# Kernel optimization log

Hardware: AMD Instinct MI355X
Metric: run time of the kernel (lower is better)

## Reference

```python
import jax, jax.numpy as jnp
import numpy as np

HIDDEN = 2048
N_HEADS = 32
HEAD_DIM = HIDDEN // N_HEADS
CONV_K = 4
INTER = 5632  # 256*ceil(2048*4*2/3/256)
EPS = 1e-6


def _rms(x, w):
    return x * jax.lax.rsqrt(jnp.mean(x * x, axis=-1, keepdims=True) + EPS) * w


def _l2norm(x):
    n = jnp.sqrt(jnp.sum(x * x, axis=-1, keepdims=True))
    return x / jnp.maximum(n, 1e-12)


def _causal_dwconv(x, w):
    # x [B,T,C], w [C,K] depthwise causal conv (left pad K-1), matches conv1d(pad=K-1)[..., :T]
    C, K = w.shape
    xt = jnp.transpose(x, (0, 2, 1))  # [B,C,T]
    out = jax.lax.conv_general_dilated(
        xt, w[:, None, :], window_strides=(1,), padding=[(K - 1, 0)],
        feature_group_count=C, dimension_numbers=('NCH', 'OIH', 'NCH'))
    return jnp.transpose(out, (0, 2, 1))


def _delta_scan(k, q, v, beta):
    # k,q,v: [B,T,nh,hd]; beta: [B,T,nh]. Per-head state S [hd(v), hd(k)].
    B, T, nh, hd = k.shape
    km, qm, vm = (jnp.moveaxis(a, 1, 0) for a in (k, q, v))  # [T,B,nh,hd]
    bm = jnp.moveaxis(beta, 1, 0)  # [T,B,nh]

    def step(S, inp):
        kt, qt, vt, bt = inp
        err = jnp.einsum('bhvk,bhk->bhv', S, kt) - vt
        S = S - bt[..., None, None] * err[..., None] * kt[..., None, :]
        o = jnp.einsum('bhvk,bhk->bhv', S, qt)
        return S, o

    S0 = jnp.zeros((B, nh, hd, hd), k.dtype)
    S, o = jax.lax.scan(step, S0, (km, qm, vm, bm))
    return jnp.moveaxis(o, 0, 1), S


def setup_inputs() -> dict:
    key = jax.random.key(0)
    ks = jax.random.split(key, 12)
    s = 0.02
    d = {
        'hidden_states': jax.random.normal(ks[0], (1, 1024, HIDDEN), jnp.float32),
        'attn_norm_w': jnp.ones((HIDDEN,), jnp.float32),
        'Wq': jax.random.normal(ks[1], (HIDDEN, HIDDEN), jnp.float32) * s,
        'Wk': jax.random.normal(ks[2], (HIDDEN, HIDDEN), jnp.float32) * s,
        'Wv': jax.random.normal(ks[3], (HIDDEN, HIDDEN), jnp.float32) * s,
        'conv_q': jax.random.normal(ks[4], (HIDDEN, CONV_K), jnp.float32) * 0.1,
        'conv_k': jax.random.normal(ks[5], (HIDDEN, CONV_K), jnp.float32) * 0.1,
        'conv_v': jax.random.normal(ks[6], (HIDDEN, CONV_K), jnp.float32) * 0.1,
        'Wbeta': jax.random.normal(ks[7], (N_HEADS, HIDDEN), jnp.float32) * s,
        'out_norm_w': jnp.ones((HIDDEN,), jnp.float32),
        'Wout': jax.random.normal(ks[8], (HIDDEN, HIDDEN), jnp.float32) * s,
        'mlp_norm_w': jnp.ones((HIDDEN,), jnp.float32),
        'Wgate': jax.random.normal(ks[9], (INTER, HIDDEN), jnp.float32) * s,
        'Wup': jax.random.normal(ks[10], (INTER, HIDDEN), jnp.float32) * s,
        'Wdown': jax.random.normal(ks[11], (HIDDEN, INTER), jnp.float32) * s,
    }
    return d


def reference(hidden_states, attn_norm_w, Wq, Wk, Wv, conv_q, conv_k, conv_v,
              Wbeta, out_norm_w, Wout, mlp_norm_w, Wgate, Wup, Wdown):
    x = hidden_states
    B, T, H = x.shape
    nh, hd = N_HEADS, HEAD_DIM
    silu = jax.nn.silu

    # --- DeltaNet attention sub-block ---
    h = _rms(x, attn_norm_w)
    # proj -> causal depthwise conv -> SiLU (in conv helper) -> SiLU again (forward)
    q = silu(silu(_causal_dwconv(h @ Wq.T, conv_q)))
    k = silu(silu(_causal_dwconv(h @ Wk.T, conv_k)))
    v = silu(silu(_causal_dwconv(h @ Wv.T, conv_v)))
    q = _l2norm(q.reshape(B, T, nh, hd))
    k = _l2norm(k.reshape(B, T, nh, hd))
    v = v.reshape(B, T, nh, hd)
    beta = jax.nn.sigmoid(h @ Wbeta.T)  # [B,T,nh]

    o, memory_state = _delta_scan(k, q, v, beta)
    o = o.reshape(B, T, H)
    o = _rms(o, out_norm_w) @ Wout.T
    x = x + o

    # --- SwiGLU MLP sub-block ---
    h2 = _rms(x, mlp_norm_w)
    gate = h2 @ Wgate.T
    up = h2 @ Wup.T
    x = x + (silu(gate) * up) @ Wdown.T
    return x, memory_state
```

## Files before the change

### kernel.cpp

```cpp
#include <hip/hip_runtime.h>
#include <stdint.h>

typedef unsigned short u16;
typedef unsigned int u32;

#define T_SEQ 1024
#define HID   2048
#define NH    32
#define HD    64
#define NCHUNK 16
#define INTER 5632

typedef __attribute__((ext_vector_type(8))) short b16x8;
typedef __attribute__((ext_vector_type(4))) float f32x4;

__device__ inline float bf2f(u16 u) { union { u32 i; float f; } v; v.i = ((u32)u) << 16; return v.f; }
__device__ inline u16 f2bf(float f) {
  union { float f; u32 i; } v; v.f = f;
  u32 u = v.i;
  return (u16)((u + 0x7FFFu + ((u >> 16) & 1u)) >> 16);
}
__device__ inline float silu_f(float x) { return x / (1.f + __expf(-x)); }

typedef __attribute__((address_space(1))) const unsigned int as1_u32;
typedef __attribute__((address_space(3))) unsigned int as3_u32;
__device__ inline void gl_lds16(const void* g, void* l) {
  __builtin_amdgcn_global_load_lds((as1_u32*)g, (as3_u32*)l, 16, 0, 0);
}

__global__ __launch_bounds__(256) void k_cvt_all(
    const float* __restrict__ s0, const float* __restrict__ s1, const float* __restrict__ s2,
    const float* __restrict__ s3, const float* __restrict__ s4, const float* __restrict__ s5,
    const float* __restrict__ s6,
    u16* __restrict__ d0, u16* __restrict__ d1, u16* __restrict__ d2, u16* __restrict__ d3,
    u16* __restrict__ d4, u16* __restrict__ d5, u16* __restrict__ d6) {
  int z = blockIdx.y;
  int n4 = (z < 4) ? (HID * HID / 4) : (INTER * HID / 4);
  int i = blockIdx.x * 256 + threadIdx.x;
  if (i >= n4) return;
  const float* s = (z == 0) ? s0 : (z == 1) ? s1 : (z == 2) ? s2 : (z == 3) ? s3
                   : (z == 4) ? s4 : (z == 5) ? s5 : s6;
  u16* d = (z == 0) ? d0 : (z == 1) ? d1 : (z == 2) ? d2 : (z == 3) ? d3
           : (z == 4) ? d4 : (z == 5) ? d5 : d6;
  float4 v = ((const float4*)s)[i];
  u32 lo = (u32)f2bf(v.x) | ((u32)f2bf(v.y) << 16);
  u32 hi = (u32)f2bf(v.z) | ((u32)f2bf(v.w) << 16);
  ((uint2*)d)[i] = make_uint2(lo, hi);
}

__global__ __launch_bounds__(256) void k_rms(const float* __restrict__ x, const float* __restrict__ w,
                                             u16* __restrict__ out) {
  int row = blockIdx.x, tid = threadIdx.x;
  const float* xr = x + (size_t)row * HID;
  float4 v0 = ((const float4*)xr)[tid];
  float4 v1 = ((const float4*)xr)[tid + 256];
  float ss = v0.x * v0.x + v0.y * v0.y + v0.z * v0.z + v0.w * v0.w +
             v1.x * v1.x + v1.y * v1.y + v1.z * v1.z + v1.w * v1.w;
  for (int m = 32; m; m >>= 1) ss += __shfl_xor(ss, m, 64);
  __shared__ float wsum[4];
  if ((tid & 63) == 0) wsum[tid >> 6] = ss;
  __syncthreads();
  float tot = wsum[0] + wsum[1] + wsum[2] + wsum[3];
  float sc = rsqrtf(tot / (float)HID + 1e-6f);
  float4 w0 = ((const float4*)w)[tid];
  float4 w1 = ((const float4*)w)[tid + 256];
  u32 lo, hi;
  lo = (u32)f2bf(v0.x * sc * w0.x) | ((u32)f2bf(v0.y * sc * w0.y) << 16);
  hi = (u32)f2bf(v0.z * sc * w0.z) | ((u32)f2bf(v0.w * sc * w0.w) << 16);
  ((uint2*)out)[(size_t)row * 512 + tid] = make_uint2(lo, hi);
  lo = (u32)f2bf(v1.x * sc * w1.x) | ((u32)f2bf(v1.y * sc * w1.y) << 16);
  hi = (u32)f2bf(v1.z * sc * w1.z) | ((u32)f2bf(v1.w * sc * w1.w) << 16);
  ((uint2*)out)[(size_t)row * 512 + tid + 256] = make_uint2(lo, hi);
}

__global__ __launch_bounds__(256) void k_gemm_sk(
    const u16* __restrict__ A,
    const u16* __restrict__ B0, const u16* __restrict__ B1, const u16* __restrict__ B2,
    float* __restrict__ C0, float* __restrict__ C1, float* __restrict__ C2,
    const float* __restrict__ resid, int M, int N, int Kf, int KS, int nslice) {
  int mat = blockIdx.z / nslice, slice = blockIdx.z % nslice;
  const u16* Bp = (mat == 0) ? B0 : (mat == 1 ? B1 : B2);
  float* Cp = (mat == 0) ? C0 : (mat == 1 ? C1 : C2);
  __shared__ __align__(16) u16 As[128 * 32];
  __shared__ __align__(16) u16 Bs[128 * 32];
  int tid = threadIdx.x;
  int m0 = blockIdx.y * 128, n0 = blockIdx.x * 128;
  int lane = tid & 63, wv = tid >> 6, wr = wv >> 1, wc = wv & 1;
  int lrow = lane & 15, quad = lane >> 4;
  int lr = lane >> 2;
  int lc = (((lane & 3) ^ ((lr >> 1) & 3)) * 8);
  int xq = quad ^ ((lrow >> 1) & 3);
  f32x4 acc[4][4];
#pragma unroll
  for (int i = 0; i < 4; ++i)
#pragma unroll
    for (int j = 0; j < 4; ++j) acc[i][j] = (f32x4){0.f, 0.f, 0.f, 0.f};

  int kb = slice * KS, ke = kb + KS;
  for (int k0 = kb; k0 < ke; k0 += 32) {
    const u16* Ag = A + (size_t)(m0 + wv * 32) * Kf + k0;
    const u16* Bg = Bp + (size_t)(n0 + wv * 32) * Kf + k0;
    gl_lds16(Ag + (size_t)lr * Kf + lc,        &As[(wv * 32) * 32]);
    gl_lds16(Ag + (size_t)(16 + lr) * Kf + lc, &As[(wv * 32 + 16) * 32]);
    gl_lds16(Bg + (size_t)lr * Kf + lc,        &Bs[(wv * 32) * 32]);
    gl_lds16(Bg + (size_t)(16 + lr) * Kf + lc, &Bs[(wv * 32 + 16) * 32]);
    __syncthreads();
    b16x8 af[4], bfr[4];
#pragma unroll
    for (int i = 0; i < 4; ++i) af[i] = *(const b16x8*)&As[(wr * 64 + i * 16 + lrow) * 32 + xq * 8];
#pragma unroll
    for (int j = 0; j < 4; ++j) bfr[j] = *(const b16x8*)&Bs[(wc * 64 + j * 16 + lrow) * 32 + xq * 8];
#pragma unroll
    for (int i = 0; i < 4; ++i)
#pragma unroll
      for (int j = 0; j < 4; ++j)
        acc[i][j] = __builtin_amdgcn_mfma_f32_16x16x32_bf16(af[i], bfr[j], acc[i][j], 0, 0, 0);
    __syncthreads();
  }
#pragma unroll
  for (int i = 0; i < 4; ++i)
#pragma unroll
    for (int j = 0; j < 4; ++j)
#pragma unroll
      for (int r = 0; r < 4; ++r) {
        int row = m0 + wr * 64 + i * 16 + quad * 4 + r;
        int col = n0 + wc * 64 + j * 16 + lrow;
        float val = acc[i][j][r];
        if (slice == 0 && resid) val += resid[(size_t)row * N + col];
        atomicAdd(&Cp[(size_t)row * N + col], val);
      }
}

__global__ __launch_bounds__(256) void k_gemm_gu(
    const u16* __restrict__ A, const u16* __restrict__ Bg, const u16* __restrict__ Bu,
    u16* __restrict__ D) {
  __shared__ __align__(16) u16 As[128 * 32];
  __shared__ __align__(16) u16 Gs[128 * 32];
  __shared__ __align__(16) u16 Us[128 * 32];
  int tid = threadIdx.x;
  int m0 = blockIdx.y * 128, n0 = blockIdx.x * 128;
  int lane = tid & 63, wv = tid >> 6, wr = wv >> 1, wc = wv & 1;
  int lrow = lane & 15, quad = lane >> 4;
  int lr = lane >> 2;
  int lc = (((lane & 3) ^ ((lr >> 1) & 3)) * 8);
  int xq = quad ^ ((lrow >> 1) & 3);
  f32x4 ag[4][4], au[4][4];
#pragma unroll
  for (int i = 0; i < 4; ++i)
#pragma unroll
    for (int j = 0; j < 4; ++j) { ag[i][j] = (f32x4){0.f, 0.f, 0.f, 0.f}; au[i][j] = (f32x4){0.f, 0.f, 0.f, 0.f}; }

  for (int k0 = 0; k0 < HID; k0 += 32) {
    const u16* Ap = A + (size_t)(m0 + wv * 32) * HID + k0;
    const u16* Gp = Bg + (size_t)(n0 + wv * 32) * HID + k0;
    const u16* Up = Bu + (size_t)(n0 + wv * 32) * HID + k0;
    gl_lds16(Ap + (size_t)lr * HID + lc,        &As[(wv * 32) * 32]);
    gl_lds16(Ap + (size_t)(16 + lr) * HID + lc, &As[(wv * 32 + 16) * 32]);
    gl_lds16(Gp + (size_t)lr * HID + lc,        &Gs[(wv * 32) * 32]);
    gl_lds16(Gp + (size_t)(16 + lr) * HID + lc, &Gs[(wv * 32 + 16) * 32]);
    gl_lds16(Up + (size_t)lr * HID + lc,        &Us[(wv * 32) * 32]);
    gl_lds16(Up + (size_t)(16 + lr) * HID + lc, &Us[(wv * 32 + 16) * 32]);
    __syncthreads();
    b16x8 af[4], gf[4], uf[4];
#pragma unroll
    for (int i = 0; i < 4; ++i) af[i] = *(const b16x8*)&As[(wr * 64 + i * 16 + lrow) * 32 + xq * 8];
#pragma unroll
    for (int j = 0; j < 4; ++j) gf[j] = *(const b16x8*)&Gs[(wc * 64 + j * 16 + lrow) * 32 + xq * 8];
#pragma unroll
    for (int j = 0; j < 4; ++j) uf[j] = *(const b16x8*)&Us[(wc * 64 + j * 16 + lrow) * 32 + xq * 8];
#pragma unroll
    for (int i = 0; i < 4; ++i)
#pragma unroll
      for (int j = 0; j < 4; ++j) {
        ag[i][j] = __builtin_amdgcn_mfma_f32_16x16x32_bf16(af[i], gf[j], ag[i][j], 0, 0, 0);
        au[i][j] = __builtin_amdgcn_mfma_f32_16x16x32_bf16(af[i], uf[j], au[i][j], 0, 0, 0);
      }
    __syncthreads();
  }
#pragma unroll
  for (int i = 0; i < 4; ++i)
#pragma unroll
    for (int j = 0; j < 4; ++j)
#pragma unroll
      for (int r = 0; r < 4; ++r) {
        int row = m0 + wr * 64 + i * 16 + quad * 4 + r;
        int col = n0 + wc * 64 + j * 16 + lrow;
        D[(size_t)row * INTER + col] = f2bf(silu_f(ag[i][j][r]) * au[i][j][r]);
      }
}

__global__ __launch_bounds__(256) void k_beta(const u16* __restrict__ hbf, const float* __restrict__ Wb,
                                              float* __restrict__ beta) {
  __shared__ __align__(16) float hr[HID];
  __shared__ float red[256];
  int t = blockIdx.x, tid = threadIdx.x;
#pragma unroll
  for (int i = 0; i < 8; ++i) {
    int c = i * 256 + tid;
    hr[c] = bf2f(hbf[(size_t)t * HID + c]);
  }
  __syncthreads();
  int head = tid >> 3, j = tid & 7;
  const float* wrow = Wb + (size_t)head * HID + j * 256;
  const float* hs = hr + j * 256;
  float acc = 0.f;
#pragma unroll 16
  for (int c = 0; c < 256; c += 4) {
    float4 wv = *(const float4*)&wrow[c];
    float4 hv = *(const float4*)&hs[c];
    acc += hv.x * wv.x + hv.y * wv.y + hv.z * wv.z + hv.w * wv.w;
  }
  red[tid] = acc;
  __syncthreads();
  if (tid < 32) {
    float s = 0.f;
#pragma unroll
    for (int i = 0; i < 8; ++i) s += red[tid * 8 + i];
    beta[(size_t)t * NH + tid] = 1.f / (1.f + __expf(-s));
  }
}

__global__ __launch_bounds__(256) void k_conv(const float* __restrict__ proj,
                                              const float* __restrict__ cw0, const float* __restrict__ cw1,
                                              const float* __restrict__ cw2, float* __restrict__ outp) {
  int z = blockIdx.z;
  const float* src = proj + (size_t)z * T_SEQ * HID;
  float* dst = outp + (size_t)z * T_SEQ * HID;
  const float* cw = (z == 0) ? cw0 : (z == 1 ? cw1 : cw2);
  bool l2 = (z < 2);
  int c = threadIdx.x & 63, wr = threadIdx.x >> 6;
  int head = blockIdx.y;
  int ch = head * 64 + c;
  int t0 = blockIdx.x * 64 + wr * 16;
  float4 w = ((const float4*)cw)[ch];
  float xm3 = (t0 >= 3) ? src[(size_t)(t0 - 3) * HID + ch] : 0.f;
  float xm2 = (t0 >= 2) ? src[(size_t)(t0 - 2) * HID + ch] : 0.f;
  float xm1 = (t0 >= 1) ? src[(size_t)(t0 - 1) * HID + ch] : 0.f;
  for (int i = 0; i < 16; ++i) {
    int t = t0 + i;
    float x0 = src[(size_t)t * HID + ch];
    float zv = xm3 * w.x + xm2 * w.y + xm1 * w.z + x0 * w.w;
    float s = silu_f(silu_f(zv));
    if (l2) {
      float ss = s * s;
      for (int m = 32; m; m >>= 1) ss += __shfl_xor(ss, m, 64);
      float n = sqrtf(ss);
      s = s / fmaxf(n, 1e-12f);
    }
    dst[(size_t)t * HID + ch] = s;
    xm3 = xm2; xm2 = xm1; xm1 = x0;
  }
}

__global__ __launch_bounds__(256) void k_phaseA(
    const float* __restrict__ qp, const float* __restrict__ kp, const float* __restrict__ vp,
    const float* __restrict__ beta,
    u16* __restrict__ negWbf, u16* __restrict__ Uvbf, u16* __restrict__ Ktbf,
    u16* __restrict__ Qbf, u16* __restrict__ Pbf) {
  int cx = blockIdx.x, h = blockIdx.y;
  __shared__ __align__(16) u16 Kst[64 * 72];
  __shared__ __align__(16) u16 Qst[64 * 72];
  __shared__ __align__(16) float Af[64 * 68];
  __shared__ float bet[64];
  int tid = threadIdx.x;
  int t0 = cx * 64;
#pragma unroll
  for (int i = 0; i < 16; ++i) {
    int idx = i * 256 + tid, s = idx >> 6, d = idx & 63;
    size_t g = (size_t)(t0 + s) * HID + h * 64 + d;
    Kst[s * 72 + d] = f2bf(kp[g]);
    Qst[s * 72 + d] = f2bf(qp[g]);
  }
  if (tid < 64) bet[tid] = beta[(size_t)(t0 + tid) * NH + h];
  __syncthreads();
  int lane = tid & 63, wv = tid >> 6, lrow = lane & 15, quad = lane >> 4;
  f32x4 accA[4], accP[4];
#pragma unroll
  for (int i = 0; i < 4; ++i) { accA[i] = (f32x4){0.f, 0.f, 0.f, 0.f}; accP[i] = (f32x4){0.f, 0.f, 0.f, 0.f}; }
#pragma unroll
  for (int ks = 0; ks < 2; ++ks) {
    b16x8 bk = *(const b16x8*)&Kst[(wv * 16 + lrow) * 72 + ks * 32 + quad * 8];
#pragma unroll
    for (int i = 0; i < 4; ++i) {
      b16x8 ak = *(const b16x8*)&Kst[(i * 16 + lrow) * 72 + ks * 32 + quad * 8];
      b16x8 aq = *(const b16x8*)&Qst[(i * 16 + lrow) * 72 + ks * 32 + quad * 8];
      accA[i] = __builtin_amdgcn_mfma_f32_16x16x32_bf16(ak, bk, accA[i], 0, 0, 0);
      accP[i] = __builtin_amdgcn_mfma_f32_16x16x32_bf16(aq, bk, accP[i], 0, 0, 0);
    }
  }
  size_t cb2 = ((size_t)h * NCHUNK + cx) * 4096;
#pragma unroll
  for (int i = 0; i < 4; ++i)
#pragma unroll
    for (int r = 0; r < 4; ++r) {
      int srow = i * 16 + quad * 4 + r, col = wv * 16 + lrow;
      Af[srow * 68 + col] = (col < srow) ? accA[i][r] * bet[srow] : 0.f;
      Pbf[cb2 + srow * 64 + col] = f2bf((col <= srow) ? accP[i][r] : 0.f);
    }
  __syncthreads();
  if (wv < 2) {
    int c = lane;
    float x[64];
    if (wv == 0) {
#pragma unroll
      for (int s = 0; s < 64; ++s) x[s] = bet[s] * bf2f(Kst[s * 72 + c]);
    } else {
#pragma unroll
      for (int s = 0; s < 64; ++s) x[s] = bet[s] * vp[(size_t)(t0 + s) * HID + h * 64 + c];
    }
#pragma unroll
    for (int s = 1; s < 64; ++s) {
      float a = 0.f;
#pragma unroll
      for (int r = 0; r < (s & ~3); r += 4) {
        float4 av = *(const float4*)&Af[s * 68 + r];
        a += av.x * x[r] + av.y * x[r + 1] + av.z * x[r + 2] + av.w * x[r + 3];
      }
#pragma unroll
      for (int r = (s & ~3); r < s; ++r) a += Af[s * 68 + r] * x[r];
      x[s] -= a;
    }
    if (wv == 0) {
#pragma unroll
      for (int s = 0; s < 64; ++s) negWbf[cb2 + s * 64 + c] = f2bf(-x[s]);
    } else {
#pragma unroll
      for (int s = 0; s < 64; ++s) Uvbf[cb2 + s * 64 + c] = f2bf(x[s]);
    }
  } else if (wv == 2) {
#pragma unroll
    for (int it = 0; it < 8; ++it) {
      int cidx = it * 64 + lane, s = cidx >> 3, d0 = (cidx & 7) * 8;
      *(uint4*)&Qbf[cb2 + s * 64 + d0] = *(const uint4*)&Qst[s * 72 + d0];
    }
  } else {
#pragma unroll
    for (int it = 0; it < 8; ++it) {
      int cidx = it * 64 + lane, d = cidx >> 3, s0 = (cidx & 7) * 8;
      u16 tmp[8];
#pragma unroll
      for (int j = 0; j < 8; ++j) tmp[j] = Kst[(s0 + j) * 72 + d];
      *(uint4*)&Ktbf[cb2 + d * 64 + s0] = *(const uint4*)tmp;
    }
  }
}

__global__ __launch_bounds__(256) void k_phaseB1(
    const u16* __restrict__ negWbf, const u16* __restrict__ Uvbf, const u16* __restrict__ Ktbf,
    u16* __restrict__ Utws, u16* __restrict__ Sws, float* __restrict__ Sout) {
  int h = blockIdx.x, tid = threadIdx.x;
  __shared__ __align__(16) u16 S0b[2][64 * 72];
  __shared__ __align__(16) u16 Ut[64 * 72];
  int lane = tid & 63, wv = tid >> 6, lrow = lane & 15, quad = lane >> 4;
#pragma unroll
  for (int i = 0; i < 16; ++i) {
    int idx = i * 256 + tid;
    S0b[0][(idx >> 6) * 72 + (idx & 63)] = 0;
  }
  f32x4 aS[4];
#pragma unroll
  for (int i = 0; i < 4; ++i) aS[i] = (f32x4){0.f, 0.f, 0.f, 0.f};

  b16x8 Wf[2][4][2]; b16x8 Ktf[2][2]; u16 Uvr[2][4][4];
  size_t hb = (size_t)h * NCHUNK * 4096;
  {
    size_t cb2 = hb;
#pragma unroll
    for (int i = 0; i < 4; ++i)
#pragma unroll
      for (int ks = 0; ks < 2; ++ks)
        Wf[0][i][ks] = *(const b16x8*)&negWbf[cb2 + (i * 16 + lrow) * 64 + ks * 32 + quad * 8];
#pragma unroll
    for (int ks = 0; ks < 2; ++ks)
      Ktf[0][ks] = *(const b16x8*)&Ktbf[cb2 + (wv * 16 + lrow) * 64 + ks * 32 + quad * 8];
#pragma unroll
    for (int i = 0; i < 4; ++i)
#pragma unroll
      for (int r = 0; r < 4; ++r)
        Uvr[0][i][r] = Uvbf[cb2 + (i * 16 + quad * 4 + r) * 64 + wv * 16 + lrow];
  }
  __syncthreads();
#pragma unroll
  for (int cx = 0; cx < NCHUNK; ++cx) {
    const int p = cx & 1, q = p ^ 1;
    size_t cb2 = hb + (size_t)cx * 4096;
    if (cx > 0) {
#pragma unroll
      for (int i = 0; i < 2; ++i) {
        int cidx = i * 256 + tid, dv = cidx >> 3, s0 = (cidx & 7) * 8;
        *(uint4*)&Sws[cb2 + dv * 64 + s0] = *(const uint4*)&S0b[p][dv * 72 + s0];
      }
    }
    if (cx + 1 < NCHUNK) {
      size_t cbn = cb2 + 4096;
#pragma unroll
      for (int i = 0; i < 4; ++i)
#pragma unroll
        for (int ks = 0; ks < 2; ++ks)
          Wf[q][i][ks] = *(const b16x8*)&negWbf[cbn + (i * 16 + lrow) * 64 + ks * 32 + quad * 8];
#pragma unroll
      for (int ks = 0; ks < 2; ++ks)
        Ktf[q][ks] = *(const b16x8*)&Ktbf[cbn + (wv * 16 + lrow) * 64 + ks * 32 + quad * 8];
#pragma unroll
      for (int i = 0; i < 4; ++i)
#pragma unroll
        for (int r = 0; r < 4; ++r)
          Uvr[q][i][r] = Uvbf[cbn + (i * 16 + quad * 4 + r) * 64 + wv * 16 + lrow];
    }
    f32x4 aU[4];
#pragma unroll
    for (int i = 0; i < 4; ++i)
#pragma unroll
      for (int r = 0; r < 4; ++r) aU[i][r] = bf2f(Uvr[p][i][r]);
#pragma unroll
    for (int ks = 0; ks < 2; ++ks) {
      b16x8 bS = *(const b16x8*)&S0b[p][(wv * 16 + lrow) * 72 + ks * 32 + quad * 8];
#pragma unroll
      for (int i = 0; i < 4; ++i)
        aU[i] = __builtin_amdgcn_mfma_f32_16x16x32_bf16(Wf[p][i][ks], bS, aU[i], 0, 0, 0);
    }
#pragma unroll
    for (int i = 0; i < 4; ++i)
#pragma unroll
      for (int r = 0; r < 4; ++r) {
        int s = i * 16 + quad * 4 + r, dv = wv * 16 + lrow;
        Ut[dv * 72 + s] = f2bf(aU[i][r]);
      }
    __syncthreads();
#pragma unroll
    for (int i = 0; i < 2; ++i) {
      int cidx = i * 256 + tid, dv = cidx >> 3, s0 = (cidx & 7) * 8;
      *(uint4*)&Utws[cb2 + dv * 64 + s0] = *(const uint4*)&Ut[dv * 72 + s0];
    }
#pragma unroll
    for (int ks = 0; ks < 2; ++ks) {
#pragma unroll
      for (int i = 0; i < 4; ++i) {
        b16x8 a = *(const b16x8*)&Ut[(i * 16 + lrow) * 72 + ks * 32 + quad * 8];
        aS[i] = __builtin_amdgcn_mfma_f32_16x16x32_bf16(a, Ktf[p][ks], aS[i], 0, 0, 0);
      }
    }
#pragma unroll
    for (int i = 0; i < 4; ++i)
#pragma unroll
      for (int r = 0; r < 4; ++r) {
        int dv = i * 16 + quad * 4 + r, dk = wv * 16 + lrow;
        S0b[q][dv * 72 + dk] = f2bf(aS[i][r]);
      }
    __syncthreads();
  }
#pragma unroll
  for (int i = 0; i < 4; ++i)
#pragma unroll
    for (int r = 0; r < 4; ++r) {
      int dv = i * 16 + quad * 4 + r, dk = wv * 16 + lrow;
      Sout[(size_t)h * 4096 + dv * 64 + dk] = aS[i][r];
    }
}

__global__ __launch_bounds__(256) void k_phaseB2(
    const u16* __restrict__ Qbf, const u16* __restrict__ Pbf,
    const u16* __restrict__ Utws, const u16* __restrict__ Sws, float* __restrict__ o) {
  int cx = blockIdx.x, h = blockIdx.y, tid = threadIdx.x;
  int lane = tid & 63, wv = tid >> 6, lrow = lane & 15, quad = lane >> 4;
  size_t cb2 = ((size_t)h * NCHUNK + cx) * 4096;
  f32x4 aO[4];
#pragma unroll
  for (int i = 0; i < 4; ++i) aO[i] = (f32x4){0.f, 0.f, 0.f, 0.f};
#pragma unroll
  for (int ks = 0; ks < 2; ++ks) {
    b16x8 Uf = *(const b16x8*)&Utws[cb2 + (wv * 16 + lrow) * 64 + ks * 32 + quad * 8];
#pragma unroll
    for (int i = 0; i < 4; ++i) {
      b16x8 Pf = *(const b16x8*)&Pbf[cb2 + (i * 16 + lrow) * 64 + ks * 32 + quad * 8];
      aO[i] = __builtin_amdgcn_mfma_f32_16x16x32_bf16(Pf, Uf, aO[i], 0, 0, 0);
    }
  }
  if (cx > 0) {
#pragma unroll
    for (int ks = 0; ks < 2; ++ks) {
      b16x8 Sf = *(const b16x8*)&Sws[cb2 + (wv * 16 + lrow) * 64 + ks * 32 + quad * 8];
#pragma unroll
      for (int i = 0; i < 4; ++i) {
        b16x8 Qf = *(const b16x8*)&Qbf[cb2 + (i * 16 + lrow) * 64 + ks * 32 + quad * 8];
        aO[i] = __builtin_amdgcn_mfma_f32_16x16x32_bf16(Qf, Sf, aO[i], 0, 0, 0);
      }
    }
  }
  int t0 = cx * 64;
#pragma unroll
  for (int i = 0; i < 4; ++i)
#pragma unroll
    for (int r = 0; r < 4; ++r)
      o[(size_t)(t0 + i * 16 + quad * 4 + r) * HID + h * 64 + wv * 16 + lrow] = aO[i][r];
}

extern "C" void kernel_launch(void* const* d_in, const int* in_sizes, int n_in,
                              void* d_out, int out_size, void* d_ws, size_t ws_size,
                              hipStream_t stream) {
  const float* x     = (const float*)d_in[0];
  const float* anw   = (const float*)d_in[1];
  const float* Wq    = (const float*)d_in[2];
  const float* Wk    = (const float*)d_in[3];
  const float* Wv    = (const float*)d_in[4];
  const float* convq = (const float*)d_in[5];
  const float* convk = (const float*)d_in[6];
  const float* convv = (const float*)d_in[7];
  const float* Wbeta = (const float*)d_in[8];
  const float* onw   = (const float*)d_in[9];
  const float* Wout  = (const float*)d_in[10];
  const float* mnw   = (const float*)d_in[11];
  const float* Wgate = (const float*)d_in[12];
  const float* Wup   = (const float*)d_in[13];
  const float* Wdown = (const float*)d_in[14];
  float* out = (float*)d_out;

  const size_t TH = (size_t)T_SEQ * HID;
  const size_t SCAN = (size_t)NH * NCHUNK * 4096;
  char* wsb = (char*)d_ws;
  size_t off = 0;
  auto alloc = [&](size_t bytes) -> void* {
    void* p = wsb + off;
    off += (bytes + 255) & ~(size_t)255;
    return p;
  };
  u16* wq_bf    = (u16*)alloc((size_t)HID * HID * 2);
  u16* wk_bf    = (u16*)alloc((size_t)HID * HID * 2);
  u16* wv_bf    = (u16*)alloc((size_t)HID * HID * 2);
  u16* wout_bf  = (u16*)alloc((size_t)HID * HID * 2);
  u16* wgate_bf = (u16*)alloc((size_t)INTER * HID * 2);
  u16* wup_bf   = (u16*)alloc((size_t)INTER * HID * 2);
  u16* wdown_bf = (u16*)alloc((size_t)HID * INTER * 2);
  u16* actbf    = (u16*)alloc(TH * 2);
  float* qkv_proj = (float*)alloc(3 * TH * 4);
  float* qkvpost  = (float*)alloc(3 * TH * 4);
  float* betab    = (float*)alloc((size_t)T_SEQ * NH * 4);
  u16* negWbf = (u16*)alloc(SCAN * 2);
  u16* Uvbf   = (u16*)alloc(SCAN * 2);
  u16* Ktbf   = (u16*)alloc(SCAN * 2);
  u16* Qbf    = (u16*)alloc(SCAN * 2);
  u16* Pbf    = (u16*)alloc(SCAN * 2);
  u16* Utws   = (u16*)alloc(SCAN * 2);
  u16* Sws    = (u16*)alloc(SCAN * 2);
  float* x1   = (float*)alloc(TH * 4);
  float* obuf = qkv_proj;
  u16* g_bf   = negWbf;

  k_cvt_all<<<dim3(INTER * HID / 4 / 256, 7), 256, 0, stream>>>(
      Wq, Wk, Wv, Wout, Wgate, Wup, Wdown,
      wq_bf, wk_bf, wv_bf, wout_bf, wgate_bf, wup_bf, wdown_bf);

  k_rms<<<dim3(T_SEQ), 256, 0, stream>>>(x, anw, actbf);
  hipMemsetAsync(qkv_proj, 0, 3 * TH * 4, stream);
  k_gemm_sk<<<dim3(HID / 128, T_SEQ / 128, 6), 256, 0, stream>>>(
      actbf, wq_bf, wk_bf, wv_bf, qkv_proj, qkv_proj + TH, qkv_proj + 2 * TH, nullptr,
      T_SEQ, HID, HID, HID / 2, 2);
  k_beta<<<dim3(T_SEQ), 256, 0, stream>>>(actbf, Wbeta, betab);
  k_conv<<<dim3(T_SEQ / 64, NH, 3), 256, 0, stream>>>(qkv_proj, convq, convk, convv, qkvpost);
  k_phaseA<<<dim3(NCHUNK, NH), 256, 0, stream>>>(
      qkvpost, qkvpost + TH, qkvpost + 2 * TH, betab, negWbf, Uvbf, Ktbf, Qbf, Pbf);
  k_phaseB1<<<dim3(NH), 256, 0, stream>>>(negWbf, Uvbf, Ktbf, Utws, Sws, out + TH);
  k_phaseB2<<<dim3(NCHUNK, NH), 256, 0, stream>>>(Qbf, Pbf, Utws, Sws, obuf);
  k_rms<<<dim3(T_SEQ), 256, 0, stream>>>(obuf, onw, actbf);
  hipMemsetAsync(x1, 0, TH * 4, stream);
  k_gemm_sk<<<dim3(HID / 128, T_SEQ / 128, 4), 256, 0, stream>>>(
      actbf, wout_bf, wout_bf, wout_bf, x1, x1, x1, x, T_SEQ, HID, HID, HID / 4, 4);
  k_rms<<<dim3(T_SEQ), 256, 0, stream>>>(x1, mnw, actbf);
  k_gemm_gu<<<dim3(INTER / 128, T_SEQ / 128), 256, 0, stream>>>(actbf, wgate_bf, wup_bf, g_bf);
  hipMemsetAsync(out, 0, TH * 4, stream);
  k_gemm_sk<<<dim3(HID / 128, T_SEQ / 128, 4), 256, 0, stream>>>(
      g_bf, wdown_bf, wdown_bf, wdown_bf, out, out, out, x1, T_SEQ, HID, INTER, INTER / 4, 4);
}
```

Measured before the change: 706.3 us.

## Double-buffer LDS in GEMM kernels and remap gate/up blocks across XCDs

Both MFMA GEMM kernels now keep two LDS buffers and issue the global-to-LDS loads for the next K tile before computing on the current one, leaving one barrier per iteration. The aim is to hide load latency behind MFMA work. The gate/up GEMM is launched as a flat 1D grid whose block index is remapped so neighbouring XCDs get different N tiles and share the same activation rows; surplus blocks exit early. The three accumulator memsets are moved to the start of the stream. Double buffering doubles LDS use (48KB for gate/up), which may lower occupancy.

```diff
diff --git a/kernel.cpp b/kernel.cpp
--- a/kernel.cpp
+++ b/kernel.cpp
@@ -81,8 +81,8 @@
   int mat = blockIdx.z / nslice, slice = blockIdx.z % nslice;
   const u16* Bp = (mat == 0) ? B0 : (mat == 1 ? B1 : B2);
   float* Cp = (mat == 0) ? C0 : (mat == 1 ? C1 : C2);
-  __shared__ __align__(16) u16 As[128 * 32];
-  __shared__ __align__(16) u16 Bs[128 * 32];
+  __shared__ __align__(16) u16 As[2][128 * 32];
+  __shared__ __align__(16) u16 Bs[2][128 * 32];
   int tid = threadIdx.x;
   int m0 = blockIdx.y * 128, n0 = blockIdx.x * 128;
   int lane = tid & 63, wv = tid >> 6, wr = wv >> 1, wc = wv & 1;
@@ -96,20 +96,26 @@
 #pragma unroll
     for (int j = 0; j < 4; ++j) acc[i][j] = (f32x4){0.f, 0.f, 0.f, 0.f};
 
-  int kb = slice * KS, ke = kb + KS;
-  for (int k0 = kb; k0 < ke; k0 += 32) {
-    const u16* Ag = A + (size_t)(m0 + wv * 32) * Kf + k0;
-    const u16* Bg = Bp + (size_t)(n0 + wv * 32) * Kf + k0;
-    gl_lds16(Ag + (size_t)lr * Kf + lc,        &As[(wv * 32) * 32]);
-    gl_lds16(Ag + (size_t)(16 + lr) * Kf + lc, &As[(wv * 32 + 16) * 32]);
-    gl_lds16(Bg + (size_t)lr * Kf + lc,        &Bs[(wv * 32) * 32]);
-    gl_lds16(Bg + (size_t)(16 + lr) * Kf + lc, &Bs[(wv * 32 + 16) * 32]);
-    __syncthreads();
+  const u16* Agb = A + (size_t)(m0 + wv * 32 + lr) * Kf + lc;
+  const u16* Bgb = Bp + (size_t)(n0 + wv * 32 + lr) * Kf + lc;
+  auto stage = [&](int k0, int b) {
+    gl_lds16(Agb + k0,                     &As[b][(wv * 32) * 32]);
+    gl_lds16(Agb + (size_t)16 * Kf + k0,   &As[b][(wv * 32 + 16) * 32]);
+    gl_lds16(Bgb + k0,                     &Bs[b][(wv * 32) * 32]);
+    gl_lds16(Bgb + (size_t)16 * Kf + k0,   &Bs[b][(wv * 32 + 16) * 32]);
+  };
+  int kb = slice * KS;
+  int nIt = KS / 32;
+  stage(kb, 0);
+  __syncthreads();
+  for (int it = 0; it < nIt; ++it) {
+    int p = it & 1;
+    if (it + 1 < nIt) stage(kb + (it + 1) * 32, p ^ 1);
     b16x8 af[4], bfr[4];
 #pragma unroll
-    for (int i = 0; i < 4; ++i) af[i] = *(const b16x8*)&As[(wr * 64 + i * 16 + lrow) * 32 + xq * 8];
-#pragma unroll
-    for (int j = 0; j < 4; ++j) bfr[j] = *(const b16x8*)&Bs[(wc * 64 + j * 16 + lrow) * 32 + xq * 8];
+    for (int i = 0; i < 4; ++i) af[i] = *(const b16x8*)&As[p][(wr * 64 + i * 16 + lrow) * 32 + xq * 8];
+#pragma unroll
+    for (int j = 0; j < 4; ++j) bfr[j] = *(const b16x8*)&Bs[p][(wc * 64 + j * 16 + lrow) * 32 + xq * 8];
 #pragma unroll
     for (int i = 0; i < 4; ++i)
 #pragma unroll
@@ -134,11 +140,15 @@
 __global__ __launch_bounds__(256) void k_gemm_gu(
     const u16* __restrict__ A, const u16* __restrict__ Bg, const u16* __restrict__ Bu,
     u16* __restrict__ D) {
-  __shared__ __align__(16) u16 As[128 * 32];
-  __shared__ __align__(16) u16 Gs[128 * 32];
-  __shared__ __align__(16) u16 Us[128 * 32];
+  int flat = blockIdx.x;
+  int xcd = flat & 7, idx = flat >> 3;
+  int n = xcd + 8 * (idx >> 3), m = idx & 7;
+  if (n >= INTER / 128) return;
+  __shared__ __align__(16) u16 As[2][128 * 32];
+  __shared__ __align__(16) u16 Gs[2][128 * 32];
+  __shared__ __align__(16) u16 Us[2][128 * 32];
   int tid = threadIdx.x;
-  int m0 = blockIdx.y * 128, n0 = blockIdx.x * 128;
+  int m0 = m * 128, n0 = n * 128;
   int lane = tid & 63, wv = tid >> 6, wr = wv >> 1, wc = wv & 1;
   int lrow = lane & 15, quad = lane >> 4;
   int lr = lane >> 2;
@@ -150,24 +160,29 @@
 #pragma unroll
     for (int j = 0; j < 4; ++j) { ag[i][j] = (f32x4){0.f, 0.f, 0.f, 0.f}; au[i][j] = (f32x4){0.f, 0.f, 0.f, 0.f}; }
 
-  for (int k0 = 0; k0 < HID; k0 += 32) {
-    const u16* Ap = A + (size_t)(m0 + wv * 32) * HID + k0;
-    const u16* Gp = Bg + (size_t)(n0 + wv * 32) * HID + k0;
-    const u16* Up = Bu + (size_t)(n0 + wv * 32) * HID + k0;
-    gl_lds16(Ap + (size_t)lr * HID + lc,        &As[(wv * 32) * 32]);
-    gl_lds16(Ap + (size_t)(16 + lr) * HID + lc, &As[(wv * 32 + 16) * 32]);
-    gl_lds16(Gp + (size_t)lr * HID + lc,        &Gs[(wv * 32) * 32]);
-    gl_lds16(Gp + (size_t)(16 + lr) * HID + lc, &Gs[(wv * 32 + 16) * 32]);
-    gl_lds16(Up + (size_t)lr * HID + lc,        &Us[(wv * 32) * 32]);
-    gl_lds16(Up + (size_t)(16 + lr) * HID + lc, &Us[(wv * 32 + 16) * 32]);
-    __syncthreads();
+  const u16* Agb = A + (size_t)(m0 + wv * 32 + lr) * HID + lc;
+  const u16* Ggb = Bg + (size_t)(n0 + wv * 32 + lr) * HID + lc;
+  const u16* Ugb = Bu + (size_t)(n0 + wv * 32 + lr) * HID + lc;
+  auto stage = [&](int k0, int b) {
+    gl_lds16(Agb + k0,                    &As[b][(wv * 32) * 32]);
+    gl_lds16(Agb + (size_t)16 * HID + k0, &As[b][(wv * 32 + 16) * 32]);
+    gl_lds16(Ggb + k0,                    &Gs[b][(wv * 32) * 32]);
+    gl_lds16(Ggb + (size_t)16 * HID + k0, &Gs[b][(wv * 32 + 16) * 32]);
+    gl_lds16(Ugb + k0,                    &Us[b][(wv * 32) * 32]);
+    gl_lds16(Ugb + (size_t)16 * HID + k0, &Us[b][(wv * 32 + 16) * 32]);
+  };
+  stage(0, 0);
+  __syncthreads();
+  for (int it = 0; it < HID / 32; ++it) {
+    int p = it & 1;
+    if (it + 1 < HID / 32) stage((it + 1) * 32, p ^ 1);
     b16x8 af[4], gf[4], uf[4];
 #pragma unroll
-    for (int i = 0; i < 4; ++i) af[i] = *(const b16x8*)&As[(wr * 64 + i * 16 + lrow) * 32 + xq * 8];
-#pragma unroll
-    for (int j = 0; j < 4; ++j) gf[j] = *(const b16x8*)&Gs[(wc * 64 + j * 16 + lrow) * 32 + xq * 8];
-#pragma unroll
-    for (int j = 0; j < 4; ++j) uf[j] = *(const b16x8*)&Us[(wc * 64 + j * 16 + lrow) * 32 + xq * 8];
+    for (int i = 0; i < 4; ++i) af[i] = *(const b16x8*)&As[p][(wr * 64 + i * 16 + lrow) * 32 + xq * 8];
+#pragma unroll
+    for (int j = 0; j < 4; ++j) gf[j] = *(const b16x8*)&Gs[p][(wc * 64 + j * 16 + lrow) * 32 + xq * 8];
+#pragma unroll
+    for (int j = 0; j < 4; ++j) uf[j] = *(const b16x8*)&Us[p][(wc * 64 + j * 16 + lrow) * 32 + xq * 8];
 #pragma unroll
     for (int i = 0; i < 4; ++i)
 #pragma unroll
@@ -546,12 +561,15 @@
   float* obuf = qkv_proj;
   u16* g_bf   = negWbf;
 
+  hipMemsetAsync(qkv_proj, 0, 3 * TH * 4, stream);
+  hipMemsetAsync(x1, 0, TH * 4, stream);
+  hipMemsetAsync(out, 0, TH * 4, stream);
+
   k_cvt_all<<<dim3(INTER * HID / 4 / 256, 7), 256, 0, stream>>>(
       Wq, Wk, Wv, Wout, Wgate, Wup, Wdown,
       wq_bf, wk_bf, wv_bf, wout_bf, wgate_bf, wup_bf, wdown_bf);
 
   k_rms<<<dim3(T_SEQ), 256, 0, stream>>>(x, anw, actbf);
-  hipMemsetAsync(qkv_proj, 0, 3 * TH * 4, stream);
   k_gemm_sk<<<dim3(HID / 128, T_SEQ / 128, 6), 256, 0, stream>>>(
       actbf, wq_bf, wk_bf, wv_bf, qkv_proj, qkv_proj + TH, qkv_proj + 2 * TH, nullptr,
       T_SEQ, HID, HID, HID / 2, 2);
@@ -562,12 +580,10 @@
   k_phaseB1<<<dim3(NH), 256, 0, stream>>>(negWbf, Uvbf, Ktbf, Utws, Sws, out + TH);
   k_phaseB2<<<dim3(NCHUNK, NH), 256, 0, stream>>>(Qbf, Pbf, Utws, Sws, obuf);
   k_rms<<<dim3(T_SEQ), 256, 0, stream>>>(obuf, onw, actbf);
-  hipMemsetAsync(x1, 0, TH * 4, stream);
   k_gemm_sk<<<dim3(HID / 128, T_SEQ / 128, 4), 256, 0, stream>>>(
       actbf, wout_bf, wout_bf, wout_bf, x1, x1, x1, x, T_SEQ, HID, HID, HID / 4, 4);
   k_rms<<<dim3(T_SEQ), 256, 0, stream>>>(x1, mnw, actbf);
-  k_gemm_gu<<<dim3(INTER / 128, T_SEQ / 128), 256, 0, stream>>>(actbf, wgate_bf, wup_bf, g_bf);
-  hipMemsetAsync(out, 0, TH * 4, stream);
+  k_gemm_gu<<<dim3(384), 256, 0, stream>>>(actbf, wgate_bf, wup_bf, g_bf);
   k_gemm_sk<<<dim3(HID / 128, T_SEQ / 128, 4), 256, 0, stream>>>(
       g_bf, wdown_bf, wdown_bf, wdown_bf, out, out, out, x1, T_SEQ, HID, INTER, INTER / 4, 4);
 }
```

Result: faster. 659.4 us (-6.6%).

## Load GEMM MFMA fragments directly from global memory, dropping LDS staging and barriers

Applied to the files above, without the earlier changes.

The split-K and gate/up GEMMs no longer stage tiles through LDS with global_load_lds and barriers. Each lane now loads its MFMA operand fragments straight from global memory into registers. The split-K kernel uses a templated, fully unrolled K loop with register double-buffering. The gate/up GEMM gets a flattened 1D grid with an XCD-aware block swizzle so blocks sharing weight columns land on the same XCD. The three memsets are also moved to the start of the stream. The aim is to remove LDS round-trips and block synchronisation, at the cost of redundant global/L2 loads across waves, narrower per-row accesses, and higher register pressure from full unrolling.

```diff
diff --git a/kernel.cpp b/kernel.cpp
--- a/kernel.cpp
+++ b/kernel.cpp
@@ -21,12 +21,6 @@
   return (u16)((u + 0x7FFFu + ((u >> 16) & 1u)) >> 16);
 }
 __device__ inline float silu_f(float x) { return x / (1.f + __expf(-x)); }
-
-typedef __attribute__((address_space(1))) const unsigned int as1_u32;
-typedef __attribute__((address_space(3))) unsigned int as3_u32;
-__device__ inline void gl_lds16(const void* g, void* l) {
-  __builtin_amdgcn_global_load_lds((as1_u32*)g, (as3_u32*)l, 16, 0, 0);
-}
 
 __global__ __launch_bounds__(256) void k_cvt_all(
     const float* __restrict__ s0, const float* __restrict__ s1, const float* __restrict__ s2,
@@ -73,49 +67,54 @@
   ((uint2*)out)[(size_t)row * 512 + tid + 256] = make_uint2(lo, hi);
 }
 
+template <int NIT>
 __global__ __launch_bounds__(256) void k_gemm_sk(
     const u16* __restrict__ A,
     const u16* __restrict__ B0, const u16* __restrict__ B1, const u16* __restrict__ B2,
     float* __restrict__ C0, float* __restrict__ C1, float* __restrict__ C2,
-    const float* __restrict__ resid, int M, int N, int Kf, int KS, int nslice) {
+    const float* __restrict__ resid, int N, int Kf, int nslice) {
   int mat = blockIdx.z / nslice, slice = blockIdx.z % nslice;
   const u16* Bp = (mat == 0) ? B0 : (mat == 1 ? B1 : B2);
   float* Cp = (mat == 0) ? C0 : (mat == 1 ? C1 : C2);
-  __shared__ __align__(16) u16 As[128 * 32];
-  __shared__ __align__(16) u16 Bs[128 * 32];
   int tid = threadIdx.x;
   int m0 = blockIdx.y * 128, n0 = blockIdx.x * 128;
   int lane = tid & 63, wv = tid >> 6, wr = wv >> 1, wc = wv & 1;
   int lrow = lane & 15, quad = lane >> 4;
-  int lr = lane >> 2;
-  int lc = (((lane & 3) ^ ((lr >> 1) & 3)) * 8);
-  int xq = quad ^ ((lrow >> 1) & 3);
+  int kb = slice * (NIT * 32);
+  const u16* Ar[4];
+  const u16* Br[4];
+#pragma unroll
+  for (int i = 0; i < 4; ++i) {
+    Ar[i] = A + (size_t)(m0 + wr * 64 + i * 16 + lrow) * Kf + kb + quad * 8;
+    Br[i] = Bp + (size_t)(n0 + wc * 64 + i * 16 + lrow) * Kf + kb + quad * 8;
+  }
   f32x4 acc[4][4];
 #pragma unroll
   for (int i = 0; i < 4; ++i)
 #pragma unroll
     for (int j = 0; j < 4; ++j) acc[i][j] = (f32x4){0.f, 0.f, 0.f, 0.f};
 
-  int kb = slice * KS, ke = kb + KS;
-  for (int k0 = kb; k0 < ke; k0 += 32) {
-    const u16* Ag = A + (size_t)(m0 + wv * 32) * Kf + k0;
-    const u16* Bg = Bp + (size_t)(n0 + wv * 32) * Kf + k0;
-    gl_lds16(Ag + (size_t)lr * Kf + lc,        &As[(wv * 32) * 32]);
-    gl_lds16(Ag + (size_t)(16 + lr) * Kf + lc, &As[(wv * 32 + 16) * 32]);
-    gl_lds16(Bg + (size_t)lr * Kf + lc,        &Bs[(wv * 32) * 32]);
-    gl_lds16(Bg + (size_t)(16 + lr) * Kf + lc, &Bs[(wv * 32 + 16) * 32]);
-    __syncthreads();
-    b16x8 af[4], bfr[4];
-#pragma unroll
-    for (int i = 0; i < 4; ++i) af[i] = *(const b16x8*)&As[(wr * 64 + i * 16 + lrow) * 32 + xq * 8];
-#pragma unroll
-    for (int j = 0; j < 4; ++j) bfr[j] = *(const b16x8*)&Bs[(wc * 64 + j * 16 + lrow) * 32 + xq * 8];
+  b16x8 af[2][4], bfr[2][4];
+#pragma unroll
+  for (int i = 0; i < 4; ++i) {
+    af[0][i] = *(const b16x8*)(Ar[i]);
+    bfr[0][i] = *(const b16x8*)(Br[i]);
+  }
+#pragma unroll
+  for (int it = 0; it < NIT; ++it) {
+    const int p = it & 1;
+    if (it + 1 < NIT) {
+#pragma unroll
+      for (int i = 0; i < 4; ++i) {
+        af[p ^ 1][i] = *(const b16x8*)(Ar[i] + (it + 1) * 32);
+        bfr[p ^ 1][i] = *(const b16x8*)(Br[i] + (it + 1) * 32);
+      }
+    }
 #pragma unroll
     for (int i = 0; i < 4; ++i)
 #pragma unroll
       for (int j = 0; j < 4; ++j)
-        acc[i][j] = __builtin_amdgcn_mfma_f32_16x16x32_bf16(af[i], bfr[j], acc[i][j], 0, 0, 0);
-    __syncthreads();
+        acc[i][j] = __builtin_amdgcn_mfma_f32_16x16x32_bf16(af[p][i], bfr[p][j], acc[i][j], 0, 0, 0);
   }
 #pragma unroll
   for (int i = 0; i < 4; ++i)
@@ -134,40 +133,38 @@
 __global__ __launch_bounds__(256) void k_gemm_gu(
     const u16* __restrict__ A, const u16* __restrict__ Bg, const u16* __restrict__ Bu,
     u16* __restrict__ D) {
-  __shared__ __align__(16) u16 As[128 * 32];
-  __shared__ __align__(16) u16 Gs[128 * 32];
-  __shared__ __align__(16) u16 Us[128 * 32];
+  int flat = blockIdx.x;
+  int xcd = flat & 7, idx = flat >> 3;
+  int n = xcd + 8 * (idx >> 3), m = idx & 7;
+  if (n >= INTER / 128) return;
   int tid = threadIdx.x;
-  int m0 = blockIdx.y * 128, n0 = blockIdx.x * 128;
+  int m0 = m * 128, n0 = n * 128;
   int lane = tid & 63, wv = tid >> 6, wr = wv >> 1, wc = wv & 1;
   int lrow = lane & 15, quad = lane >> 4;
-  int lr = lane >> 2;
-  int lc = (((lane & 3) ^ ((lr >> 1) & 3)) * 8);
-  int xq = quad ^ ((lrow >> 1) & 3);
+  const u16* Ar[4];
+  const u16* Gr[4];
+  const u16* Ur[4];
+#pragma unroll
+  for (int i = 0; i < 4; ++i) {
+    Ar[i] = A + (size_t)(m0 + wr * 64 + i * 16 + lrow) * HID + quad * 8;
+    Gr[i] = Bg + (size_t)(n0 + wc * 64 + i * 16 + lrow) * HID + quad * 8;
+    Ur[i] = Bu + (size_t)(n0 + wc * 64 + i * 16 + lrow) * HID + quad * 8;
+  }
   f32x4 ag[4][4], au[4][4];
 #pragma unroll
   for (int i = 0; i < 4; ++i)
 #pragma unroll
     for (int j = 0; j < 4; ++j) { ag[i][j] = (f32x4){0.f, 0.f, 0.f, 0.f}; au[i][j] = (f32x4){0.f, 0.f, 0.f, 0.f}; }
 
-  for (int k0 = 0; k0 < HID; k0 += 32) {
-    const u16* Ap = A + (size_t)(m0 + wv * 32) * HID + k0;
-    const u16* Gp = Bg + (size_t)(n0 + wv * 32) * HID + k0;
-    const u16* Up = Bu + (size_t)(n0 + wv * 32) * HID + k0;
-    gl_lds16(Ap + (size_t)lr * HID + lc,        &As[(wv * 32) * 32]);
-    gl_lds16(Ap + (size_t)(16 + lr) * HID + lc, &As[(wv * 32 + 16) * 32]);
-    gl_lds16(Gp + (size_t)lr * HID + lc,        &Gs[(wv * 32) * 32]);
-    gl_lds16(Gp + (size_t)(16 + lr) * HID + lc, &Gs[(wv * 32 + 16) * 32]);
-    gl_lds16(Up + (size_t)lr * HID + lc,        &Us[(wv * 32) * 32]);
-    gl_lds16(Up + (size_t)(16 + lr) * HID + lc, &Us[(wv * 32 + 16) * 32]);
-    __syncthreads();
+#pragma unroll
+  for (int it = 0; it < HID / 32; ++it) {
     b16x8 af[4], gf[4], uf[4];
 #pragma unroll
-    for (int i = 0; i < 4; ++i) af[i] = *(const b16x8*)&As[(wr * 64 + i * 16 + lrow) * 32 + xq * 8];
-#pragma unroll
-    for (int j = 0; j < 4; ++j) gf[j] = *(const b16x8*)&Gs[(wc * 64 + j * 16 + lrow) * 32 + xq * 8];
-#pragma unroll
-    for (int j = 0; j < 4; ++j) uf[j] = *(const b16x8*)&Us[(wc * 64 + j * 16 + lrow) * 32 + xq * 8];
+    for (int i = 0; i < 4; ++i) {
+      af[i] = *(const b16x8*)(Ar[i] + it * 32);
+      gf[i] = *(const b16x8*)(Gr[i] + it * 32);
+      uf[i] = *(const b16x8*)(Ur[i] + it * 32);
+    }
 #pragma unroll
     for (int i = 0; i < 4; ++i)
 #pragma unroll
@@ -175,7 +172,6 @@
         ag[i][j] = __builtin_amdgcn_mfma_f32_16x16x32_bf16(af[i], gf[j], ag[i][j], 0, 0, 0);
         au[i][j] = __builtin_amdgcn_mfma_f32_16x16x32_bf16(af[i], uf[j], au[i][j], 0, 0, 0);
       }
-    __syncthreads();
   }
 #pragma unroll
   for (int i = 0; i < 4; ++i)
@@ -546,15 +542,18 @@
   float* obuf = qkv_proj;
   u16* g_bf   = negWbf;
 
+  hipMemsetAsync(qkv_proj, 0, 3 * TH * 4, stream);
+  hipMemsetAsync(x1, 0, TH * 4, stream);
+  hipMemsetAsync(out, 0, TH * 4, stream);
+
   k_cvt_all<<<dim3(INTER * HID / 4 / 256, 7), 256, 0, stream>>>(
       Wq, Wk, Wv, Wout, Wgate, Wup, Wdown,
       wq_bf, wk_bf, wv_bf, wout_bf, wgate_bf, wup_bf, wdown_bf);
 
   k_rms<<<dim3(T_SEQ), 256, 0, stream>>>(x, anw, actbf);
-  hipMemsetAsync(qkv_proj, 0, 3 * TH * 4, stream);
-  k_gemm_sk<<<dim3(HID / 128, T_SEQ / 128, 6), 256, 0, stream>>>(
+  k_gemm_sk<32><<<dim3(HID / 128, T_SEQ / 128, 6), 256, 0, stream>>>(
       actbf, wq_bf, wk_bf, wv_bf, qkv_proj, qkv_proj + TH, qkv_proj + 2 * TH, nullptr,
-      T_SEQ, HID, HID, HID / 2, 2);
+      HID, HID, 2);
   k_beta<<<dim3(T_SEQ), 256, 0, stream>>>(actbf, Wbeta, betab);
   k_conv<<<dim3(T_SEQ / 64, NH, 3), 256, 0, stream>>>(qkv_proj, convq, convk, convv, qkvpost);
   k_phaseA<<<dim3(NCHUNK, NH), 256, 0, stream>>>(
@@ -562,12 +561,10 @@
   k_phaseB1<<<dim3(NH), 256, 0, stream>>>(negWbf, Uvbf, Ktbf, Utws, Sws, out + TH);
   k_phaseB2<<<dim3(NCHUNK, NH), 256, 0, stream>>>(Qbf, Pbf, Utws, Sws, obuf);
   k_rms<<<dim3(T_SEQ), 256, 0, stream>>>(obuf, onw, actbf);
-  hipMemsetAsync(x1, 0, TH * 4, stream);
-  k_gemm_sk<<<dim3(HID / 128, T_SEQ / 128, 4), 256, 0, stream>>>(
-      actbf, wout_bf, wout_bf, wout_bf, x1, x1, x1, x, T_SEQ, HID, HID, HID / 4, 4);
+  k_gemm_sk<16><<<dim3(HID / 128, T_SEQ / 128, 4), 256, 0, stream>>>(
+      actbf, wout_bf, wout_bf, wout_bf, x1, x1, x1, x, HID, HID, 4);
   k_rms<<<dim3(T_SEQ), 256, 0, stream>>>(x1, mnw, actbf);
-  k_gemm_gu<<<dim3(INTER / 128, T_SEQ / 128), 256, 0, stream>>>(actbf, wgate_bf, wup_bf, g_bf);
-  hipMemsetAsync(out, 0, TH * 4, stream);
-  k_gemm_sk<<<dim3(HID / 128, T_SEQ / 128, 4), 256, 0, stream>>>(
-      g_bf, wdown_bf, wdown_bf, wdown_bf, out, out, out, x1, T_SEQ, HID, INTER, INTER / 4, 4);
-}
+  k_gemm_gu<<<dim3(384), 256, 0, stream>>>(actbf, wgate_bf, wup_bf, g_bf);
+  k_gemm_sk<44><<<dim3(HID / 128, T_SEQ / 128, 4), 256, 0, stream>>>(
+      g_bf, wdown_bf, wdown_bf, wdown_bf, out, out, out, x1, HID, INTER, 4);
+}
```

Measured after the change: 864.4 us. 1.22x slower.
